# Kernel optimization log

Measured on AMD Instinct MI355X. Metric: run time of the kernel, lower is better.

## Reference

```python
import jax, jax.numpy as jnp
import numpy as np
import math

H, M, N = 64, 128, 128  # volume dims (m == n required by original index math)
K_NEIGH = 9
W_WIN = 3


def build_neighbor_ids(h, n, w):
    # Periodic (wrap-around) neighbor indices, matching extract_neighbour_indices
    # with m == n. Loop order: z-major, then y, then x, offsets -1..1 for w=3.
    half = w // 2
    offs = list(range(-half, half + 1))
    zi = jnp.arange(h)[:, None, None]
    yi = jnp.arange(n)[None, :, None]
    xi = jnp.arange(n)[None, None, :]
    cols = []
    for oz in offs:
        for oy in offs:
            for ox in offs:
                idx = ((zi + oz) % h) * (n * n) + ((yi + oy) % n) * n + ((xi + ox) % n)
                cols.append(idx.reshape(-1))
    return jnp.stack(cols, axis=1).astype(jnp.int32)  # [P, w^3]


def setup_inputs() -> dict:
    key = jax.random.key(0)
    k1, _ = jax.random.split(key)
    inp = jax.random.normal(k1, (H, M, N), dtype=jnp.float32)
    ksigma = jnp.ones((1, 1, 1, 1), dtype=jnp.float32)  # nn.Parameter init to sigma_m=1.0
    return {"input": inp, "ksigma": ksigma, "k": K_NEIGH, "w": W_WIN}


def reference(input, ksigma, k, w):
    h, m, n = input.shape
    ID = build_neighbor_ids(h, n, w)               # [P, nN]
    anat = input.reshape(-1)                       # [P]
    # get_knn: absolute intensity differences to each neighbor
    dist = jnp.abs(anat[ID] - anat[:, None])       # [P, nN]
    order = jnp.argsort(dist, axis=-1, stable=True)
    sID = jnp.take_along_axis(ID, order, axis=1)   # sorted neighbor indices
    IDk = sID[:, :k]                               # [P, k] top-k nearest by intensity
    Wk = anat[IDk]                                 # [P, k] neighbor intensities (feature rows)
    # get_features: per-row std (torch.std is unbiased, ddof=1)
    sigma = jnp.std(Wk, axis=1, ddof=1)            # [P]
    sigma_safe = jnp.where(sigma == 0, 1.0, sigma)
    neigh = Wk[IDk]                                # [P, k, k] gather feature rows of knn
    diff = Wk[:, None, :] - neigh + 1e-6           # pairwise_distance eps added to diff
    norm = jnp.sqrt(jnp.sum(diff * diff, axis=-1)) # [P, k] L2 pairwise distance
    ks = ksigma.reshape(())
    logits = -jnp.square(norm / sigma_safe[:, None] / (math.sqrt(2.0) * ks))
    logits = jnp.where(sigma[:, None] == 0, 0.0, logits)  # zero row -> uniform softmax
    Kw = jax.nn.softmax(logits, axis=1)            # [P, k] normalized kernel weights
    return Kw
```

## Files before the change

kernel.cpp:

```cpp
#include <hip/hip_runtime.h>
#include <hip/hip_fp16.h>
#include <array>

constexpr int HZ   = 64;
constexpr int NN   = 128;
constexpr int P    = HZ * NN * NN;
constexpr int KSEL = 9;
constexpr int NCOL = 27;

typedef _Float16 f16x2 __attribute__((ext_vector_type(2)));

constexpr int TY = 10;
constexpr int TX = 34;
constexpr int TROWS = 3 * TY * TX;

constexpr int compute_nce(int n) {
  int t = 0; while ((1 << t) < n) ++t;
  int cnt = 0;
  for (int p = 1 << (t - 1); p > 0; p >>= 1) {
    int q = 1 << (t - 1), r = 0, d = p;
    while (true) {
      for (int i = 0; i < n - d; ++i)
        if ((i & p) == r) ++cnt;
      if (q == p) break;
      d = q - p; r = p; q >>= 1;
    }
  }
  return cnt;
}
constexpr int NCE_FULL = compute_nce(NCOL);

struct CEPair { unsigned char a, b; };
constexpr std::array<CEPair, NCE_FULL> make_net() {
  std::array<CEPair, NCE_FULL> net{};
  int t = 0; while ((1 << t) < NCOL) ++t;
  int k = 0;
  for (int p = 1 << (t - 1); p > 0; p >>= 1) {
    int q = 1 << (t - 1), r = 0, d = p;
    while (true) {
      for (int i = 0; i < NCOL - d; ++i)
        if ((i & p) == r) {
          net[k].a = (unsigned char)i;
          net[k].b = (unsigned char)(i + d);
          ++k;
        }
      if (q == p) break;
      d = q - p; r = p; q >>= 1;
    }
  }
  return net;
}
constexpr auto FULLNET = make_net();

constexpr int count_pruned() {
  bool needed[NCOL] = {};
  for (int i = 0; i < KSEL; ++i) needed[i] = true;
  int cnt = 0;
  for (int e = NCE_FULL - 1; e >= 0; --e) {
    const int a = FULLNET[e].a, b = FULLNET[e].b;
    if (needed[a] || needed[b]) { needed[a] = true; needed[b] = true; ++cnt; }
  }
  return cnt;
}
constexpr int NCE = count_pruned();

constexpr std::array<CEPair, NCE> make_pruned() {
  bool needed[NCOL] = {};
  for (int i = 0; i < KSEL; ++i) needed[i] = true;
  std::array<bool, NCE_FULL> keep{};
  for (int e = NCE_FULL - 1; e >= 0; --e) {
    const int a = FULLNET[e].a, b = FULLNET[e].b;
    if (needed[a] || needed[b]) { keep[e] = true; needed[a] = true; needed[b] = true; }
  }
  std::array<CEPair, NCE> out{};
  int k = 0;
  for (int e = 0; e < NCE_FULL; ++e) if (keep[e]) out[k++] = FULLNET[e];
  return out;
}
constexpr auto NET = make_pruned();

typedef const __attribute__((address_space(1))) unsigned GU;
typedef __attribute__((address_space(3))) unsigned LU;

__device__ __forceinline__ void g2l16(const void* g, void* l) {
  __builtin_amdgcn_global_load_lds((GU*)g, (LU*)l, 16, 0, 0);
}
__device__ __forceinline__ void g2l4(const void* g, void* l) {
  __builtin_amdgcn_global_load_lds((GU*)g, (LU*)l, 4, 0, 0);
}

__global__ __launch_bounds__(256) void topk9(
    const float* __restrict__ anat,
    uint4* __restrict__ rowsA,
    unsigned* __restrict__ rowsB0,
    unsigned* __restrict__ rowsB1) {
  __shared__ float in_t[TROWS];
  const int tid = threadIdx.x;

  const int blk = blockIdx.x;
  const int swz = ((blk & 7) << 9) | (blk >> 3);
  const int z    = swz >> 6;
  const int rest = swz & 63;
  const int y0   = ((rest >> 2) & 15) << 3;
  const int x0   = (rest & 3) << 5;
  const int xl   = tid & 31;
  const int yl   = tid >> 5;

  #pragma unroll
  for (int s = 0; s < 4; ++s) {
    const unsigned q = (unsigned)(s * 256 + tid);
    if (q < (unsigned)TROWS) {
      const unsigned p = q / TX;
      const unsigned r = q - p * TX;
      const unsigned pz = p / TY;
      const int zi = (int)pz, yi = (int)(p - TY * pz);
      const int zz = (z + zi - 1) & (HZ - 1);
      const int yy = (y0 + yi - 1) & (NN - 1);
      const int xg = (x0 - 1 + (int)r) & (NN - 1);
      g2l4(&anat[(zz << 14) | (yy << 7) | xg], &in_t[q]);
    }
  }
  __syncthreads();

  const int base = (yl * TX) + xl;
  const float center = in_t[base + 1 * (TY * TX) + 1 * TX + 1];

  unsigned long long key[NCOL];
  #pragma unroll
  for (int c = 0; c < NCOL; ++c) {
    const int czi = c / 9, cyi = (c / 3) % 3, cxi = c % 3;
    const float v = in_t[base + czi * (TY * TX) + cyi * TX + cxi];
    const unsigned vb = __float_as_uint(v);
    const unsigned db = __float_as_uint(v - center) & 0x7fffffffu;
    const unsigned lo32 = ((unsigned)c << 27) | (vb >> 5);
    key[c] = ((unsigned long long)db << 32) | lo32;
  }

  #pragma unroll
  for (int e = 0; e < NCE; ++e) {
    const int a = NET[e].a, b = NET[e].b;
    const double ka = __builtin_bit_cast(double, key[a]);
    const double kb = __builtin_bit_cast(double, key[b]);
    key[a] = __builtin_bit_cast(unsigned long long, fmin(ka, kb));
    key[b] = __builtin_bit_cast(unsigned long long, fmax(ka, kb));
  }

  unsigned od[4] = {0, 0, 0, 0};
  unsigned h8 = 0, lo = 0, hi = 0;
  #pragma unroll
  for (int s = 0; s < KSEL; ++s) {
    const unsigned kl = (unsigned)key[s];
    const unsigned c  = (kl >> 27) & 31u;
    const unsigned vbits = (kl & 0x07ffffffu) << 5;
    const unsigned hb = (unsigned)__half_as_ushort(__float2half(__uint_as_float(vbits)));
    if (s < 8) od[s >> 1] |= hb << ((s & 1) * 16);
    else       h8 = hb;
    if (s < 6) lo |= c << (5 * s);
    else       hi |= c << (5 * (s - 6));
  }

  const unsigned vb = (unsigned)((z << 14) | ((y0 + yl) << 7) | (x0 + xl));
  rowsA[vb]  = make_uint4(od[0], od[1], od[2], od[3]);
  rowsB0[vb] = h8 | (hi << 16);
  rowsB1[vb] = lo;
}

__global__ __launch_bounds__(256, 5) void weights9(
    const uint4* __restrict__ rowsA,
    const unsigned* __restrict__ rowsB0,
    const unsigned* __restrict__ rowsB1,
    const float* __restrict__ ksig,
    float* __restrict__ out) {
  __shared__ unsigned tile[TROWS * 5];
  unsigned* tA  = tile;
  unsigned* tB0 = tile + TROWS * 4;
  const int tid = threadIdx.x;

  const int blk = blockIdx.x;
  const int swz = ((blk & 7) << 9) | (blk >> 3);
  const int z    = swz >> 6;
  const int rest = swz & 63;
  const int y0   = ((rest >> 2) & 15) << 3;
  const int x0   = (rest & 3) << 5;
  const int xl   = tid & 31;
  const int yl   = tid >> 5;

  const unsigned vb_own = (unsigned)((z << 14) | ((y0 + yl) << 7) | (x0 + xl));
  const unsigned lo = rowsB1[vb_own];

  #pragma unroll
  for (int s = 0; s < 4; ++s) {
    const unsigned q = (unsigned)(s * 256 + tid);
    if (q < (unsigned)TROWS) {
      const unsigned p = q / TX;
      const unsigned r = q - p * TX;
      const unsigned pz = p / TY;
      const int zi = (int)pz, yi = (int)(p - TY * pz);
      const int zz = (z + zi - 1) & (HZ - 1);
      const int yy = (y0 + yi - 1) & (NN - 1);
      const int xg = (x0 - 1 + (int)r) & (NN - 1);
      const unsigned vb = (unsigned)((zz << 14) | (yy << 7) | xg);
      g2l16(&rowsA[vb],  &tA[q * 4]);
      g2l4 (&rowsB0[vb], &tB0[q]);
    }
  }
  __syncthreads();

  const int rho_own = (TY + (yl + 1)) * TX + (xl + 1);
  const uint4 a = *(const uint4*)&tA[rho_own * 4];
  const unsigned b0 = tB0[rho_own];
  f16x2 wh[5];
  wh[0] = __builtin_bit_cast(f16x2, a.x);
  wh[1] = __builtin_bit_cast(f16x2, a.y);
  wh[2] = __builtin_bit_cast(f16x2, a.z);
  wh[3] = __builtin_bit_cast(f16x2, a.w);
  wh[4] = __builtin_bit_cast(f16x2, b0 & 0xffffu);
  const unsigned hi = b0 >> 16;

  int rho[KSEL];
  #pragma unroll
  for (int j = 0; j < KSEL; ++j) {
    const unsigned c = (j < 6) ? ((lo >> (5 * j)) & 31u)
                               : ((hi >> (5 * (j - 6))) & 31u);
    const unsigned czi = (c * 57u) >> 9;
    const unsigned rem = c - 9u * czi;
    const unsigned cyi = (rem * 11u) >> 5;
    const unsigned cxi = rem - 3u * cyi;
    rho[j] = (int)czi * (TY * TX) + (yl + (int)cyi) * TX + (xl + (int)cxi);
  }
  uint4 na[KSEL];
  unsigned nb[KSEL];
  #pragma unroll
  for (int j = 0; j < KSEL; ++j) {
    na[j] = *(const uint4*)&tA[rho[j] * 4];
    nb[j] = tB0[rho[j]];
  }

  float ws[KSEL];
  #pragma unroll
  for (int l = 0; l < KSEL; ++l) ws[l] = (float)wh[l >> 1][l & 1];
  float mean = 0.f;
  #pragma unroll
  for (int l = 0; l < KSEL; ++l) mean += ws[l];
  mean *= (1.0f / 9.0f);
  float var = 0.f;
  #pragma unroll
  for (int l = 0; l < KSEL; ++l) { const float t = ws[l] - mean; var += t * t; }
  var *= (1.0f / 8.0f);
  const float sigma = sqrtf(var);

  const float ks = ksig[0];
  const float inv = (sigma == 0.f) ? 0.f : 1.0f / (2.0f * ks * ks * sigma * sigma);

  const _Float16 epsh = (_Float16)1e-6f;
  const f16x2 eps2 = {epsh, epsh};

  float logit[KSEL];
  #pragma unroll
  for (int j = 0; j < KSEL; ++j) {
    const f16x2 nh0 = __builtin_bit_cast(f16x2, na[j].x);
    const f16x2 nh1 = __builtin_bit_cast(f16x2, na[j].y);
    const f16x2 nh2 = __builtin_bit_cast(f16x2, na[j].z);
    const f16x2 nh3 = __builtin_bit_cast(f16x2, na[j].w);
    const f16x2 nh4 = __builtin_bit_cast(f16x2, nb[j] & 0xffffu);
    float s = 0.f;
    f16x2 dd;
    dd = (wh[0] - nh0) + eps2; s = __builtin_amdgcn_fdot2(dd, dd, s, false);
    dd = (wh[1] - nh1) + eps2; s = __builtin_amdgcn_fdot2(dd, dd, s, false);
    dd = (wh[2] - nh2) + eps2; s = __builtin_amdgcn_fdot2(dd, dd, s, false);
    dd = (wh[3] - nh3) + eps2; s = __builtin_amdgcn_fdot2(dd, dd, s, false);
    dd = (wh[4] - nh4) + eps2; s = __builtin_amdgcn_fdot2(dd, dd, s, false);
    logit[j] = -s * inv;
  }

  float mx = logit[0];
  #pragma unroll
  for (int j = 1; j < KSEL; ++j) mx = fmaxf(mx, logit[j]);
  float sum = 0.f;
  float e[KSEL];
  #pragma unroll
  for (int j = 0; j < KSEL; ++j) { e[j] = __expf(logit[j] - mx); sum += e[j]; }
  const float rs = 1.0f / sum;

  __syncthreads();
  float* tf = (float*)tile;
  #pragma unroll
  for (int j = 0; j < KSEL; ++j) tf[tid * KSEL + j] = e[j] * rs;
  __syncthreads();

  const float4* tf4 = (const float4*)tile;
  #pragma unroll
  for (int s = 0; s < 3; ++s) {
    const unsigned q = (unsigned)(s * 256 + tid);
    if (q < 576u) {
      const unsigned row = q / 72u;
      const unsigned f   = q - row * 72u;
      const unsigned vb  = (unsigned)((z << 14) | ((y0 + (int)row) << 7) | x0);
      ((float4*)out)[(size_t)(vb >> 2) * 9 + f] = tf4[row * 72 + f];
    }
  }
}

extern "C" void kernel_launch(void* const* d_in, const int* in_sizes, int n_in,
                              void* d_out, int out_size, void* d_ws, size_t ws_size,
                              hipStream_t stream) {
  const float* anat = (const float*)d_in[0];
  const float* ksig = (const float*)d_in[1];
  uint4* rowsA      = (uint4*)d_ws;
  unsigned* rowsB0  = (unsigned*)d_ws + (size_t)4 * P;
  unsigned* rowsB1  = rowsB0 + P;

  const int blocks = P / 256;
  topk9<<<blocks, 256, 0, stream>>>(anat, rowsA, rowsB0, rowsB1);
  weights9<<<blocks, 256, 0, stream>>>(rowsA, rowsB0, rowsB1, ksig, (float*)d_out);
}
```

Baseline: 108.4 us.

## Replace LDS halo staging in weights kernel with direct global neighbor gathers

The weights kernel stops staging a halo tile of feature rows into shared memory and instead gathers each of the 9 selected neighbors' rows directly from global memory, relying on L2/cache reuse. The workspace layout changes to a 16-bit tail array plus a separate 8-byte index word, and output is written per thread directly instead of via an LDS transpose for coalesced float4 stores. Softmax uses exp2 with log2e folded into the scale. This removes LDS traffic, the barrier, and redundant halo loads, but adds scattered global gathers and less coalesced output stores.

```diff
diff --git a/kernel.cpp b/kernel.cpp
--- a/kernel.cpp
+++ b/kernel.cpp
@@ -82,18 +82,15 @@
 typedef const __attribute__((address_space(1))) unsigned GU;
 typedef __attribute__((address_space(3))) unsigned LU;
 
-__device__ __forceinline__ void g2l16(const void* g, void* l) {
-  __builtin_amdgcn_global_load_lds((GU*)g, (LU*)l, 16, 0, 0);
-}
 __device__ __forceinline__ void g2l4(const void* g, void* l) {
   __builtin_amdgcn_global_load_lds((GU*)g, (LU*)l, 4, 0, 0);
 }
 
-__global__ __launch_bounds__(256) void topk9(
+__global__ __launch_bounds__(256) void topk10(
     const float* __restrict__ anat,
     uint4* __restrict__ rowsA,
-    unsigned* __restrict__ rowsB0,
-    unsigned* __restrict__ rowsB1) {
+    unsigned short* __restrict__ rowsB0h,
+    uint2* __restrict__ rowsC) {
   __shared__ float in_t[TROWS];
   const int tid = threadIdx.x;
 
@@ -160,20 +157,17 @@
   }
 
   const unsigned vb = (unsigned)((z << 14) | ((y0 + yl) << 7) | (x0 + xl));
-  rowsA[vb]  = make_uint4(od[0], od[1], od[2], od[3]);
-  rowsB0[vb] = h8 | (hi << 16);
-  rowsB1[vb] = lo;
-}
-
-__global__ __launch_bounds__(256, 5) void weights9(
+  rowsA[vb]   = make_uint4(od[0], od[1], od[2], od[3]);
+  rowsB0h[vb] = (unsigned short)h8;
+  rowsC[vb]   = make_uint2(lo, hi);
+}
+
+__global__ __launch_bounds__(256, 4) void weights10(
     const uint4* __restrict__ rowsA,
-    const unsigned* __restrict__ rowsB0,
-    const unsigned* __restrict__ rowsB1,
+    const unsigned short* __restrict__ rowsB0h,
+    const uint2* __restrict__ rowsC,
     const float* __restrict__ ksig,
     float* __restrict__ out) {
-  __shared__ unsigned tile[TROWS * 5];
-  unsigned* tA  = tile;
-  unsigned* tB0 = tile + TROWS * 4;
   const int tid = threadIdx.x;
 
   const int blk = blockIdx.x;
@@ -185,39 +179,23 @@
   const int xl   = tid & 31;
   const int yl   = tid >> 5;
 
-  const unsigned vb_own = (unsigned)((z << 14) | ((y0 + yl) << 7) | (x0 + xl));
-  const unsigned lo = rowsB1[vb_own];
-
-  #pragma unroll
-  for (int s = 0; s < 4; ++s) {
-    const unsigned q = (unsigned)(s * 256 + tid);
-    if (q < (unsigned)TROWS) {
-      const unsigned p = q / TX;
-      const unsigned r = q - p * TX;
-      const unsigned pz = p / TY;
-      const int zi = (int)pz, yi = (int)(p - TY * pz);
-      const int zz = (z + zi - 1) & (HZ - 1);
-      const int yy = (y0 + yi - 1) & (NN - 1);
-      const int xg = (x0 - 1 + (int)r) & (NN - 1);
-      const unsigned vb = (unsigned)((zz << 14) | (yy << 7) | xg);
-      g2l16(&rowsA[vb],  &tA[q * 4]);
-      g2l4 (&rowsB0[vb], &tB0[q]);
-    }
-  }
-  __syncthreads();
-
-  const int rho_own = (TY + (yl + 1)) * TX + (xl + 1);
-  const uint4 a = *(const uint4*)&tA[rho_own * 4];
-  const unsigned b0 = tB0[rho_own];
+  const int y = y0 + yl;
+  const int x = x0 + xl;
+  const unsigned vb_own = (unsigned)((z << 14) | (y << 7) | x);
+
+  const uint4 a = rowsA[vb_own];
+  const unsigned h8o = (unsigned)rowsB0h[vb_own];
+  const uint2 cw = rowsC[vb_own];
+  const unsigned lo = cw.x, hi = cw.y;
+
   f16x2 wh[5];
   wh[0] = __builtin_bit_cast(f16x2, a.x);
   wh[1] = __builtin_bit_cast(f16x2, a.y);
   wh[2] = __builtin_bit_cast(f16x2, a.z);
   wh[3] = __builtin_bit_cast(f16x2, a.w);
-  wh[4] = __builtin_bit_cast(f16x2, b0 & 0xffffu);
-  const unsigned hi = b0 >> 16;
-
-  int rho[KSEL];
+  wh[4] = __builtin_bit_cast(f16x2, h8o);
+
+  unsigned vbn[KSEL];
   #pragma unroll
   for (int j = 0; j < KSEL; ++j) {
     const unsigned c = (j < 6) ? ((lo >> (5 * j)) & 31u)
@@ -226,14 +204,17 @@
     const unsigned rem = c - 9u * czi;
     const unsigned cyi = (rem * 11u) >> 5;
     const unsigned cxi = rem - 3u * cyi;
-    rho[j] = (int)czi * (TY * TX) + (yl + (int)cyi) * TX + (xl + (int)cxi);
+    const unsigned zz = (unsigned)(z + (int)czi - 1) & (HZ - 1);
+    const unsigned yy = (unsigned)(y + (int)cyi - 1) & (NN - 1);
+    const unsigned xx = (unsigned)(x + (int)cxi - 1) & (NN - 1);
+    vbn[j] = (zz << 14) | (yy << 7) | xx;
   }
   uint4 na[KSEL];
   unsigned nb[KSEL];
   #pragma unroll
   for (int j = 0; j < KSEL; ++j) {
-    na[j] = *(const uint4*)&tA[rho[j] * 4];
-    nb[j] = tB0[rho[j]];
+    na[j] = rowsA[vbn[j]];
+    nb[j] = (unsigned)rowsB0h[vbn[j]];
   }
 
   float ws[KSEL];
@@ -250,7 +231,9 @@
   const float sigma = sqrtf(var);
 
   const float ks = ksig[0];
-  const float inv = (sigma == 0.f) ? 0.f : 1.0f / (2.0f * ks * ks * sigma * sigma);
+  const float inv2 = (sigma == 0.f)
+      ? 0.f
+      : 1.4426950408889634f / (2.0f * ks * ks * sigma * sigma);
 
   const _Float16 epsh = (_Float16)1e-6f;
   const f16x2 eps2 = {epsh, epsh};
@@ -262,7 +245,7 @@
     const f16x2 nh1 = __builtin_bit_cast(f16x2, na[j].y);
     const f16x2 nh2 = __builtin_bit_cast(f16x2, na[j].z);
     const f16x2 nh3 = __builtin_bit_cast(f16x2, na[j].w);
-    const f16x2 nh4 = __builtin_bit_cast(f16x2, nb[j] & 0xffffu);
+    const f16x2 nh4 = __builtin_bit_cast(f16x2, nb[j]);
     float s = 0.f;
     f16x2 dd;
     dd = (wh[0] - nh0) + eps2; s = __builtin_amdgcn_fdot2(dd, dd, s, false);
@@ -270,7 +253,7 @@
     dd = (wh[2] - nh2) + eps2; s = __builtin_amdgcn_fdot2(dd, dd, s, false);
     dd = (wh[3] - nh3) + eps2; s = __builtin_amdgcn_fdot2(dd, dd, s, false);
     dd = (wh[4] - nh4) + eps2; s = __builtin_amdgcn_fdot2(dd, dd, s, false);
-    logit[j] = -s * inv;
+    logit[j] = -s * inv2;
   }
 
   float mx = logit[0];
@@ -279,26 +262,12 @@
   float sum = 0.f;
   float e[KSEL];
   #pragma unroll
-  for (int j = 0; j < KSEL; ++j) { e[j] = __expf(logit[j] - mx); sum += e[j]; }
+  for (int j = 0; j < KSEL; ++j) { e[j] = exp2f(logit[j] - mx); sum += e[j]; }
   const float rs = 1.0f / sum;
 
-  __syncthreads();
-  float* tf = (float*)tile;
-  #pragma unroll
-  for (int j = 0; j < KSEL; ++j) tf[tid * KSEL + j] = e[j] * rs;
-  __syncthreads();
-
-  const float4* tf4 = (const float4*)tile;
-  #pragma unroll
-  for (int s = 0; s < 3; ++s) {
-    const unsigned q = (unsigned)(s * 256 + tid);
-    if (q < 576u) {
-      const unsigned row = q / 72u;
-      const unsigned f   = q - row * 72u;
-      const unsigned vb  = (unsigned)((z << 14) | ((y0 + (int)row) << 7) | x0);
-      ((float4*)out)[(size_t)(vb >> 2) * 9 + f] = tf4[row * 72 + f];
-    }
-  }
+  float* op = out + (size_t)vb_own * 9;
+  #pragma unroll
+  for (int j = 0; j < KSEL; ++j) op[j] = e[j] * rs;
 }
 
 extern "C" void kernel_launch(void* const* d_in, const int* in_sizes, int n_in,
@@ -306,11 +275,11 @@
                               hipStream_t stream) {
   const float* anat = (const float*)d_in[0];
   const float* ksig = (const float*)d_in[1];
-  uint4* rowsA      = (uint4*)d_ws;
-  unsigned* rowsB0  = (unsigned*)d_ws + (size_t)4 * P;
-  unsigned* rowsB1  = rowsB0 + P;
+  uint4* rowsA              = (uint4*)d_ws;
+  unsigned short* rowsB0h   = (unsigned short*)((char*)d_ws + (size_t)16 * P);
+  uint2* rowsC              = (uint2*)((char*)d_ws + (size_t)18 * P);
 
   const int blocks = P / 256;
-  topk9<<<blocks, 256, 0, stream>>>(anat, rowsA, rowsB0, rowsB1);
-  weights9<<<blocks, 256, 0, stream>>>(rowsA, rowsB0, rowsB1, ksig, (float*)d_out);
-}
+  topk10<<<blocks, 256, 0, stream>>>(anat, rowsA, rowsB0h, rowsC);
+  weights10<<<blocks, 256, 0, stream>>>(rowsA, rowsB0h, rowsC, ksig, (float*)d_out);
+}
```

After: 116.3 us. +7.3%, slower.

## Vectorize halo loads and process two z-planes per block in weights kernel

Applied to the files above, without the earlier changes.

The topk kernel now loads its halo tile with 16-byte global-to-LDS transfers over an aligned 40-wide row instead of 4-byte loads. The weights kernel handles two z-slices per block, so the three-plane halo grows to four planes and the redundant halo loading per voxel drops. It also loads rowsB0 with 16-byte transfers and switches exp to exp2 with the log2(e) factor folded into the scale. In exchange, LDS use per block grows and the occupancy hint drops from 5 to 4, which may reduce latency hiding.

```diff
diff --git a/kernel.cpp b/kernel.cpp
--- a/kernel.cpp
+++ b/kernel.cpp
@@ -9,10 +9,6 @@
 constexpr int NCOL = 27;
 
 typedef _Float16 f16x2 __attribute__((ext_vector_type(2)));
-
-constexpr int TY = 10;
-constexpr int TX = 34;
-constexpr int TROWS = 3 * TY * TX;
 
 constexpr int compute_nce(int n) {
   int t = 0; while ((1 << t) < n) ++t;
@@ -85,16 +81,16 @@
 __device__ __forceinline__ void g2l16(const void* g, void* l) {
   __builtin_amdgcn_global_load_lds((GU*)g, (LU*)l, 16, 0, 0);
 }
-__device__ __forceinline__ void g2l4(const void* g, void* l) {
-  __builtin_amdgcn_global_load_lds((GU*)g, (LU*)l, 4, 0, 0);
-}
-
-__global__ __launch_bounds__(256) void topk9(
+
+constexpr int TXW = 40;
+constexpr int TPR = 30;
+
+__global__ __launch_bounds__(256) void topk11(
     const float* __restrict__ anat,
     uint4* __restrict__ rowsA,
     unsigned* __restrict__ rowsB0,
     unsigned* __restrict__ rowsB1) {
-  __shared__ float in_t[TROWS];
+  __shared__ float in_t[TPR * TXW];
   const int tid = threadIdx.x;
 
   const int blk = blockIdx.x;
@@ -107,29 +103,28 @@
   const int yl   = tid >> 5;
 
   #pragma unroll
-  for (int s = 0; s < 4; ++s) {
+  for (int s = 0; s < 2; ++s) {
     const unsigned q = (unsigned)(s * 256 + tid);
-    if (q < (unsigned)TROWS) {
-      const unsigned p = q / TX;
-      const unsigned r = q - p * TX;
-      const unsigned pz = p / TY;
-      const int zi = (int)pz, yi = (int)(p - TY * pz);
-      const int zz = (z + zi - 1) & (HZ - 1);
-      const int yy = (y0 + yi - 1) & (NN - 1);
-      const int xg = (x0 - 1 + (int)r) & (NN - 1);
-      g2l4(&anat[(zz << 14) | (yy << 7) | xg], &in_t[q]);
+    if (q < 300u) {
+      const unsigned p = q / 10u;
+      const unsigned t = q - 10u * p;
+      const unsigned zi = p / 10u;
+      const unsigned yi = p - 10u * zi;
+      const int zz = (z + (int)zi - 1) & (HZ - 1);
+      const int yy = (y0 + (int)yi - 1) & (NN - 1);
+      const int xb = (x0 - 4 + 4 * (int)t) & (NN - 1);
+      g2l16(&anat[(zz << 14) | (yy << 7) | xb], &in_t[q * 4]);
     }
   }
   __syncthreads();
 
-  const int base = (yl * TX) + xl;
-  const float center = in_t[base + 1 * (TY * TX) + 1 * TX + 1];
+  const float center = in_t[(1 * 10 + (yl + 1)) * TXW + 3 + (xl + 1)];
 
   unsigned long long key[NCOL];
   #pragma unroll
   for (int c = 0; c < NCOL; ++c) {
     const int czi = c / 9, cyi = (c / 3) % 3, cxi = c % 3;
-    const float v = in_t[base + czi * (TY * TX) + cyi * TX + cxi];
+    const float v = in_t[(czi * 10 + (yl + cyi)) * TXW + 3 + xl + cxi];
     const unsigned vb = __float_as_uint(v);
     const unsigned db = __float_as_uint(v - center) & 0x7fffffffu;
     const unsigned lo32 = ((unsigned)c << 27) | (vb >> 5);
@@ -165,137 +160,173 @@
   rowsB1[vb] = lo;
 }
 
-__global__ __launch_bounds__(256, 5) void weights9(
+constexpr int WPR  = 40;
+constexpr int WTA  = WPR * 34;
+constexpr int WTB  = WPR * TXW;
+
+__global__ __launch_bounds__(256, 4) void weights11(
     const uint4* __restrict__ rowsA,
     const unsigned* __restrict__ rowsB0,
     const unsigned* __restrict__ rowsB1,
     const float* __restrict__ ksig,
     float* __restrict__ out) {
-  __shared__ unsigned tile[TROWS * 5];
-  unsigned* tA  = tile;
-  unsigned* tB0 = tile + TROWS * 4;
+  __shared__ unsigned lds[WTA * 4 + WTB];
+  unsigned* tA  = lds;
+  unsigned* tB0 = lds + WTA * 4;
   const int tid = threadIdx.x;
 
   const int blk = blockIdx.x;
-  const int swz = ((blk & 7) << 9) | (blk >> 3);
-  const int z    = swz >> 6;
+  const int swz = ((blk & 7) << 8) | (blk >> 3);
+  const int zp   = swz >> 6;
   const int rest = swz & 63;
   const int y0   = ((rest >> 2) & 15) << 3;
   const int x0   = (rest & 3) << 5;
   const int xl   = tid & 31;
   const int yl   = tid >> 5;
-
-  const unsigned vb_own = (unsigned)((z << 14) | ((y0 + yl) << 7) | (x0 + xl));
-  const unsigned lo = rowsB1[vb_own];
-
-  #pragma unroll
-  for (int s = 0; s < 4; ++s) {
+  const int z0   = zp << 1;
+
+  const unsigned vbA = (unsigned)((z0 << 14) | ((y0 + yl) << 7) | (x0 + xl));
+  const unsigned low[2] = { rowsB1[vbA], rowsB1[vbA + (1u << 14)] };
+
+  #pragma unroll
+  for (int s = 0; s < 6; ++s) {
     const unsigned q = (unsigned)(s * 256 + tid);
-    if (q < (unsigned)TROWS) {
-      const unsigned p = q / TX;
-      const unsigned r = q - p * TX;
-      const unsigned pz = p / TY;
-      const int zi = (int)pz, yi = (int)(p - TY * pz);
-      const int zz = (z + zi - 1) & (HZ - 1);
-      const int yy = (y0 + yi - 1) & (NN - 1);
+    if (q < (unsigned)WTA) {
+      const unsigned p = q / 34u;
+      const unsigned r = q - 34u * p;
+      const unsigned zi = p / 10u;
+      const unsigned yi = p - 10u * zi;
+      const int zz = (z0 + (int)zi - 1) & (HZ - 1);
+      const int yy = (y0 + (int)yi - 1) & (NN - 1);
       const int xg = (x0 - 1 + (int)r) & (NN - 1);
-      const unsigned vb = (unsigned)((zz << 14) | (yy << 7) | xg);
-      g2l16(&rowsA[vb],  &tA[q * 4]);
-      g2l4 (&rowsB0[vb], &tB0[q]);
+      g2l16(&rowsA[(zz << 14) | (yy << 7) | xg], &tA[q * 4]);
+    }
+  }
+  #pragma unroll
+  for (int s = 0; s < 2; ++s) {
+    const unsigned q = (unsigned)(s * 256 + tid);
+    if (q < 400u) {
+      const unsigned p = q / 10u;
+      const unsigned t = q - 10u * p;
+      const unsigned zi = p / 10u;
+      const unsigned yi = p - 10u * zi;
+      const int zz = (z0 + (int)zi - 1) & (HZ - 1);
+      const int yy = (y0 + (int)yi - 1) & (NN - 1);
+      const int xb = (x0 - 4 + 4 * (int)t) & (NN - 1);
+      g2l16(&rowsB0[(zz << 14) | (yy << 7) | xb], &tB0[q * 4]);
     }
   }
   __syncthreads();
 
-  const int rho_own = (TY + (yl + 1)) * TX + (xl + 1);
-  const uint4 a = *(const uint4*)&tA[rho_own * 4];
-  const unsigned b0 = tB0[rho_own];
-  f16x2 wh[5];
-  wh[0] = __builtin_bit_cast(f16x2, a.x);
-  wh[1] = __builtin_bit_cast(f16x2, a.y);
-  wh[2] = __builtin_bit_cast(f16x2, a.z);
-  wh[3] = __builtin_bit_cast(f16x2, a.w);
-  wh[4] = __builtin_bit_cast(f16x2, b0 & 0xffffu);
-  const unsigned hi = b0 >> 16;
-
-  int rho[KSEL];
-  #pragma unroll
-  for (int j = 0; j < KSEL; ++j) {
-    const unsigned c = (j < 6) ? ((lo >> (5 * j)) & 31u)
-                               : ((hi >> (5 * (j - 6))) & 31u);
-    const unsigned czi = (c * 57u) >> 9;
-    const unsigned rem = c - 9u * czi;
-    const unsigned cyi = (rem * 11u) >> 5;
-    const unsigned cxi = rem - 3u * cyi;
-    rho[j] = (int)czi * (TY * TX) + (yl + (int)cyi) * TX + (xl + (int)cxi);
-  }
-  uint4 na[KSEL];
-  unsigned nb[KSEL];
-  #pragma unroll
-  for (int j = 0; j < KSEL; ++j) {
-    na[j] = *(const uint4*)&tA[rho[j] * 4];
-    nb[j] = tB0[rho[j]];
-  }
-
-  float ws[KSEL];
-  #pragma unroll
-  for (int l = 0; l < KSEL; ++l) ws[l] = (float)wh[l >> 1][l & 1];
-  float mean = 0.f;
-  #pragma unroll
-  for (int l = 0; l < KSEL; ++l) mean += ws[l];
-  mean *= (1.0f / 9.0f);
-  float var = 0.f;
-  #pragma unroll
-  for (int l = 0; l < KSEL; ++l) { const float t = ws[l] - mean; var += t * t; }
-  var *= (1.0f / 8.0f);
-  const float sigma = sqrtf(var);
-
   const float ks = ksig[0];
-  const float inv = (sigma == 0.f) ? 0.f : 1.0f / (2.0f * ks * ks * sigma * sigma);
-
   const _Float16 epsh = (_Float16)1e-6f;
   const f16x2 eps2 = {epsh, epsh};
 
-  float logit[KSEL];
-  #pragma unroll
-  for (int j = 0; j < KSEL; ++j) {
-    const f16x2 nh0 = __builtin_bit_cast(f16x2, na[j].x);
-    const f16x2 nh1 = __builtin_bit_cast(f16x2, na[j].y);
-    const f16x2 nh2 = __builtin_bit_cast(f16x2, na[j].z);
-    const f16x2 nh3 = __builtin_bit_cast(f16x2, na[j].w);
-    const f16x2 nh4 = __builtin_bit_cast(f16x2, nb[j] & 0xffffu);
-    float s = 0.f;
-    f16x2 dd;
-    dd = (wh[0] - nh0) + eps2; s = __builtin_amdgcn_fdot2(dd, dd, s, false);
-    dd = (wh[1] - nh1) + eps2; s = __builtin_amdgcn_fdot2(dd, dd, s, false);
-    dd = (wh[2] - nh2) + eps2; s = __builtin_amdgcn_fdot2(dd, dd, s, false);
-    dd = (wh[3] - nh3) + eps2; s = __builtin_amdgcn_fdot2(dd, dd, s, false);
-    dd = (wh[4] - nh4) + eps2; s = __builtin_amdgcn_fdot2(dd, dd, s, false);
-    logit[j] = -s * inv;
-  }
-
-  float mx = logit[0];
-  #pragma unroll
-  for (int j = 1; j < KSEL; ++j) mx = fmaxf(mx, logit[j]);
-  float sum = 0.f;
-  float e[KSEL];
-  #pragma unroll
-  for (int j = 0; j < KSEL; ++j) { e[j] = __expf(logit[j] - mx); sum += e[j]; }
-  const float rs = 1.0f / sum;
+  float res[2][9];
+
+  #pragma unroll 2
+  for (int vz = 0; vz < 2; ++vz) {
+    const unsigned lo = low[vz];
+    const int planeO = 1 + vz;
+
+    const int prO = planeO * 10 + (yl + 1);
+    const uint4 a = *(const uint4*)&tA[(prO * 34 + (xl + 1)) * 4];
+    const unsigned b0 = tB0[prO * TXW + (xl + 4)];
+    f16x2 wh[5];
+    wh[0] = __builtin_bit_cast(f16x2, a.x);
+    wh[1] = __builtin_bit_cast(f16x2, a.y);
+    wh[2] = __builtin_bit_cast(f16x2, a.z);
+    wh[3] = __builtin_bit_cast(f16x2, a.w);
+    wh[4] = __builtin_bit_cast(f16x2, b0 & 0xffffu);
+    const unsigned hi = b0 >> 16;
+
+    int rA[KSEL], rB[KSEL];
+    #pragma unroll
+    for (int j = 0; j < KSEL; ++j) {
+      const unsigned c = (j < 6) ? ((lo >> (5 * j)) & 31u)
+                                 : ((hi >> (5 * (j - 6))) & 31u);
+      const unsigned czi = (c * 57u) >> 9;
+      const unsigned rem = c - 9u * czi;
+      const unsigned cyi = (rem * 11u) >> 5;
+      const unsigned cxi = rem - 3u * cyi;
+      const int pr = (vz + (int)czi) * 10 + (yl + (int)cyi);
+      rA[j] = pr * 34 + (xl + (int)cxi);
+      rB[j] = pr * TXW + (xl + (int)cxi + 3);
+    }
+    uint4 na[KSEL];
+    unsigned nb[KSEL];
+    #pragma unroll
+    for (int j = 0; j < KSEL; ++j) {
+      na[j] = *(const uint4*)&tA[rA[j] * 4];
+      nb[j] = tB0[rB[j]];
+    }
+
+    float ws[KSEL];
+    #pragma unroll
+    for (int l = 0; l < KSEL; ++l) ws[l] = (float)wh[l >> 1][l & 1];
+    float mean = 0.f;
+    #pragma unroll
+    for (int l = 0; l < KSEL; ++l) mean += ws[l];
+    mean *= (1.0f / 9.0f);
+    float var = 0.f;
+    #pragma unroll
+    for (int l = 0; l < KSEL; ++l) { const float t = ws[l] - mean; var += t * t; }
+    var *= (1.0f / 8.0f);
+    const float sigma = sqrtf(var);
+
+    const float inv2 = (sigma == 0.f)
+        ? 0.f
+        : 1.4426950408889634f / (2.0f * ks * ks * sigma * sigma);
+
+    float logit[KSEL];
+    #pragma unroll
+    for (int j = 0; j < KSEL; ++j) {
+      const f16x2 nh0 = __builtin_bit_cast(f16x2, na[j].x);
+      const f16x2 nh1 = __builtin_bit_cast(f16x2, na[j].y);
+      const f16x2 nh2 = __builtin_bit_cast(f16x2, na[j].z);
+      const f16x2 nh3 = __builtin_bit_cast(f16x2, na[j].w);
+      const f16x2 nh4 = __builtin_bit_cast(f16x2, nb[j] & 0xffffu);
+      float s = 0.f;
+      f16x2 dd;
+      dd = (wh[0] - nh0) + eps2; s = __builtin_amdgcn_fdot2(dd, dd, s, false);
+      dd = (wh[1] - nh1) + eps2; s = __builtin_amdgcn_fdot2(dd, dd, s, false);
+      dd = (wh[2] - nh2) + eps2; s = __builtin_amdgcn_fdot2(dd, dd, s, false);
+      dd = (wh[3] - nh3) + eps2; s = __builtin_amdgcn_fdot2(dd, dd, s, false);
+      dd = (wh[4] - nh4) + eps2; s = __builtin_amdgcn_fdot2(dd, dd, s, false);
+      logit[j] = -s * inv2;
+    }
+
+    float mx = logit[0];
+    #pragma unroll
+    for (int j = 1; j < KSEL; ++j) mx = fmaxf(mx, logit[j]);
+    float sum = 0.f;
+    float e[KSEL];
+    #pragma unroll
+    for (int j = 0; j < KSEL; ++j) { e[j] = exp2f(logit[j] - mx); sum += e[j]; }
+    const float rs = 1.0f / sum;
+    #pragma unroll
+    for (int j = 0; j < KSEL; ++j) res[vz][j] = e[j] * rs;
+  }
 
   __syncthreads();
-  float* tf = (float*)tile;
-  #pragma unroll
-  for (int j = 0; j < KSEL; ++j) tf[tid * KSEL + j] = e[j] * rs;
+  float* tf = (float*)lds;
+  #pragma unroll 2
+  for (int vz = 0; vz < 2; ++vz)
+    #pragma unroll
+    for (int j = 0; j < KSEL; ++j)
+      tf[(vz * 256 + tid) * KSEL + j] = res[vz][j];
   __syncthreads();
 
-  const float4* tf4 = (const float4*)tile;
-  #pragma unroll
-  for (int s = 0; s < 3; ++s) {
+  const float4* tf4 = (const float4*)lds;
+  #pragma unroll
+  for (int s = 0; s < 5; ++s) {
     const unsigned q = (unsigned)(s * 256 + tid);
-    if (q < 576u) {
+    if (q < 1152u) {
       const unsigned row = q / 72u;
       const unsigned f   = q - row * 72u;
-      const unsigned vb  = (unsigned)((z << 14) | ((y0 + (int)row) << 7) | x0);
+      const int zz = z0 + (int)(row >> 3);
+      const int yr = (int)(row & 7u);
+      const unsigned vb = (unsigned)((zz << 14) | ((y0 + yr) << 7) | x0);
       ((float4*)out)[(size_t)(vb >> 2) * 9 + f] = tf4[row * 72 + f];
     }
   }
@@ -306,11 +337,10 @@
                               hipStream_t stream) {
   const float* anat = (const float*)d_in[0];
   const float* ksig = (const float*)d_in[1];
-  uint4* rowsA      = (uint4*)d_ws;
-  unsigned* rowsB0  = (unsigned*)d_ws + (size_t)4 * P;
-  unsigned* rowsB1  = rowsB0 + P;
-
-  const int blocks = P / 256;
-  topk9<<<blocks, 256, 0, stream>>>(anat, rowsA, rowsB0, rowsB1);
-  weights9<<<blocks, 256, 0, stream>>>(rowsA, rowsB0, rowsB1, ksig, (float*)d_out);
-}
+  uint4* rowsA     = (uint4*)d_ws;
+  unsigned* rowsB0 = (unsigned*)((char*)d_ws + (size_t)16 * P);
+  unsigned* rowsB1 = (unsigned*)((char*)d_ws + (size_t)20 * P);
+
+  topk11<<<P / 256, 256, 0, stream>>>(anat, rowsA, rowsB0, rowsB1);
+  weights11<<<P / 512, 256, 0, stream>>>(rowsA, rowsB0, rowsB1, ksig, (float*)d_out);
+}
```

Measured after the change: 109.2 us. Within noise of the previous version (+0.7%).
